# Kernel optimization log

Hardware: AMD Instinct MI355X
Metric: run time of the kernel (lower is better)

The kernel has to match this reference:

```python
import jax, jax.numpy as jnp
import numpy as np

EMBED_DIM = 1024
NUM_HEADS = 16
HEAD_DIM = EMBED_DIM // NUM_HEADS
B, L = 32, 2049
LN_EPS = 1e-5


def setup_inputs() -> dict:
    key = jax.random.key(0)
    ks = jax.random.split(key, 11)
    s = 1.0 / np.sqrt(EMBED_DIM)
    x = jax.random.normal(ks[0], (B, L, EMBED_DIM), dtype=jnp.float32)
    Wq = jax.random.normal(ks[1], (EMBED_DIM, EMBED_DIM), dtype=jnp.float32) * s
    bq = jnp.zeros((EMBED_DIM,), dtype=jnp.float32)
    Wk = jax.random.normal(ks[2], (EMBED_DIM, EMBED_DIM), dtype=jnp.float32) * s
    bk = jnp.zeros((EMBED_DIM,), dtype=jnp.float32)
    Wv = jax.random.normal(ks[3], (EMBED_DIM, EMBED_DIM), dtype=jnp.float32) * s
    bv = jnp.zeros((EMBED_DIM,), dtype=jnp.float32)
    Wo = jax.random.normal(ks[4], (EMBED_DIM, EMBED_DIM), dtype=jnp.float32) * s
    bo = jnp.zeros((EMBED_DIM,), dtype=jnp.float32)
    ln_g = jnp.ones((EMBED_DIM,), dtype=jnp.float32)
    ln_b = jnp.zeros((EMBED_DIM,), dtype=jnp.float32)
    return {"x": x, "Wq": Wq, "bq": bq, "Wk": Wk, "bk": bk, "Wv": Wv,
            "bv": bv, "Wo": Wo, "bo": bo, "ln_g": ln_g, "ln_b": ln_b}


def reference(x, Wq, bq, Wk, bk, Wv, bv, Wo, bo, ln_g, ln_b):
    # x: [B, L, D]; CLS token attends to the other L-1 tokens (dropout = eval/identity)
    cls_tok = x[:, 0, :]              # [B, D]
    others = x[:, 1:, :]              # [B, L-1, D]
    q = cls_tok @ Wq.T + bq           # [B, D]
    k = others @ Wk.T + bk            # [B, L-1, D]
    v = others @ Wv.T + bv            # [B, L-1, D]
    q = q.reshape(q.shape[0], NUM_HEADS, HEAD_DIM)                       # [B, H, d]
    k = k.reshape(k.shape[0], k.shape[1], NUM_HEADS, HEAD_DIM)           # [B, S, H, d]
    v = v.reshape(v.shape[0], v.shape[1], NUM_HEADS, HEAD_DIM)           # [B, S, H, d]
    scores = jnp.einsum('bhd,bshd->bhs', q, k) / np.sqrt(HEAD_DIM)       # [B, H, S]
    w = jax.nn.softmax(scores, axis=-1)
    attn = jnp.einsum('bhs,bshd->bhd', w, v)                             # [B, H, d]
    attn = attn.reshape(attn.shape[0], NUM_HEADS * HEAD_DIM)             # [B, D]
    out = attn @ Wo.T + bo
    y = out + cls_tok
    mu = jnp.mean(y, axis=-1, keepdims=True)
    var = jnp.var(y, axis=-1, keepdims=True)
    return (y - mu) / jnp.sqrt(var + LN_EPS) * ln_g + ln_b               # [B, D]
```

## Files before the change

### kernel.cpp

```cpp
#include <hip/hip_runtime.h>
#include <math.h>

#define B_ 32
#define L_ 2049
#define E_ 1024
#define H_ 16
#define NT_ 8
#define STILE 256
#define EC 32

#define OFF_Q     0
#define OFF_T     (OFF_Q + B_*E_)
#define OFF_QBK   (OFF_T + B_*H_*E_)
#define OFF_M     (OFF_QBK + B_*H_)
#define OFF_L     (OFF_M + B_*NT_*H_)
#define OFF_U     (OFF_L + B_*NT_*H_)
#define OFF_ATTN  (OFF_U + B_*H_*E_)
#define OFF_Y     (OFF_ATTN + B_*E_)
#define OFF_UP    (OFF_Y + B_*E_)

__global__ __launch_bounds__(256) void k_gemm32(const float* __restrict__ A, long long As, int mode,
                                                const float* __restrict__ W,
                                                const float* __restrict__ bias,
                                                const float* __restrict__ resid, long long Rs,
                                                float* __restrict__ C) {
    __shared__ float wls[2 * 1056];
    const int j0 = blockIdx.x * 2, tid = threadIdx.x;
    #pragma unroll
    for (int k = 0; k < 2; ++k) {
        int idx4 = k * 256 + tid;
        int row = idx4 >> 8, c4 = idx4 & 255;
        float4 v = *(const float4*)(W + (size_t)(j0 + row) * E_ + 4 * c4);
        *(float4*)&wls[row * 1056 + 4 * c4 + ((c4 >> 5) << 2)] = v;
    }
    __syncthreads();
    const int bb = tid >> 3, kseg = tid & 7;
    const long long kbase = (mode == 1) ? (long long)(j0 >> 6) * E_ : 0;
    const float* arow = A + (size_t)bb * As + kbase + kseg * 128;
    float a0 = 0.f, a1 = 0.f;
    #pragma unroll 4
    for (int i = 0; i < 32; ++i) {
        float4 av = *(const float4*)(arow + 4 * i);
        const float* wb = &wls[kseg * 132 + 4 * i];
        float4 w0 = *(const float4*)(wb);
        float4 w1 = *(const float4*)(wb + 1056);
        a0 += av.x * w0.x + av.y * w0.y + av.z * w0.z + av.w * w0.w;
        a1 += av.x * w1.x + av.y * w1.y + av.z * w1.z + av.w * w1.w;
    }
    #pragma unroll
    for (int off = 4; off; off >>= 1) {
        a0 += __shfl_down(a0, off, 8);
        a1 += __shfl_down(a1, off, 8);
    }
    if (kseg == 0) {
        float r0 = a0 + bias[j0], r1 = a1 + bias[j0 + 1];
        if (resid) {
            r0 += resid[(size_t)bb * Rs + j0];
            r1 += resid[(size_t)bb * Rs + j0 + 1];
        }
        C[(size_t)bb * E_ + j0] = r0;
        C[(size_t)bb * E_ + j0 + 1] = r1;
    }
}

__global__ __launch_bounds__(256) void k_tproj(const float* __restrict__ Wk,
                                               const float* __restrict__ bk,
                                               float* __restrict__ ws) {
    __shared__ float qs[64 * 33];
    __shared__ float wls[64 * 68];
    const int h = blockIdx.x, e0 = blockIdx.y * 64, tid = threadIdx.x;
    const float* q = ws + OFF_Q;
    #pragma unroll
    for (int k = 0; k < 8; ++k) {
        int idx = k * 256 + tid;
        int b = idx >> 6, d = idx & 63;
        qs[d * 33 + b] = q[(size_t)b * E_ + 64 * h + d];
    }
    #pragma unroll
    for (int k = 0; k < 4; ++k) {
        int idx4 = k * 256 + tid;
        int d = idx4 >> 4, c4 = idx4 & 15;
        float4 v = *(const float4*)(Wk + (size_t)(64 * h + d) * E_ + e0 + 4 * c4);
        *(float4*)&wls[d * 68 + 4 * c4] = v;
    }
    __syncthreads();
    const int el = tid & 63, bq8 = tid >> 6;
    float acc[8];
    #pragma unroll
    for (int i = 0; i < 8; ++i) acc[i] = 0.f;
    for (int d = 0; d < 64; ++d) {
        float wv = wls[d * 68 + el];
        #pragma unroll
        for (int i = 0; i < 8; ++i) acc[i] += qs[d * 33 + (bq8 * 8 + i)] * wv;
    }
    float* t = ws + OFF_T;
    #pragma unroll
    for (int i = 0; i < 8; ++i)
        t[((size_t)(bq8 * 8 + i) * H_ + h) * E_ + e0 + el] = acc[i] * 0.125f;
    if (e0 == 0 && tid < 32) {
        float s = 0.f;
        for (int d = 0; d < 64; ++d) s += qs[d * 33 + tid] * bk[64 * h + d];
        ws[OFF_QBK + tid * H_ + h] = s * 0.125f;
    }
}

__global__ __launch_bounds__(512) void k_attn_core(const float* __restrict__ x,
                                                   float* __restrict__ ws) {
    const int tile = blockIdx.x, b = blockIdx.y, tid = threadIdx.x;
    const int s0 = tile * STILE;
    const float* tmat = ws + OFF_T + (size_t)b * H_ * E_;
    const float* xb = x + (size_t)(b * L_ + 1 + s0) * E_;

    __shared__ float xs[18432];
    __shared__ float ts[1152];
    __shared__ float wl[STILE * 20];
    __shared__ float red[512];
    __shared__ float msh[16];

    const int lane = tid & 63;
    const int w = tid >> 6;

    float acc[16][4];
    #pragma unroll
    for (int hh = 0; hh < 16; ++hh)
        #pragma unroll
        for (int si = 0; si < 4; ++si) acc[hh][si] = 0.f;

    float4 xr[4];
    float tr;
    const int th = tid >> 5, te = tid & 31;
    {
        #pragma unroll
        for (int k = 0; k < 4; ++k) {
            int idx4 = k * 512 + tid, s = idx4 >> 3, e4 = idx4 & 7;
            xr[k] = *(const float4*)(xb + (size_t)s * E_ + 4 * e4);
        }
        tr = tmat[th * E_ + te];
        #pragma unroll
        for (int k = 0; k < 4; ++k) {
            int idx4 = k * 512 + tid, s = idx4 >> 3, e4 = idx4 & 7;
            *(float4*)&xs[s * 36 + 4 * e4] = xr[k];
        }
        ts[th * 36 + te] = tr;
    }
    for (int c = 0; c < 32; ++c) {
        __syncthreads();
        if (c + 1 < 32) {
            int ec = (c + 1) * EC;
            #pragma unroll
            for (int k = 0; k < 4; ++k) {
                int idx4 = k * 512 + tid, s = idx4 >> 3, e4 = idx4 & 7;
                xr[k] = *(const float4*)(xb + (size_t)s * E_ + ec + 4 * e4);
            }
            tr = tmat[th * E_ + ec + te];
        }
        const int bx = (c & 1) * 9216, bt = (c & 1) * 576;
        float4 xv[4];
        #pragma unroll
        for (int si = 0; si < 4; ++si)
            xv[si] = *(const float4*)&xs[bx + (lane + 64 * si) * 36 + 4 * w];
        #pragma unroll
        for (int hb = 0; hb < 4; ++hb) {
            float4 t0 = *(const float4*)&ts[bt + (4 * hb + 0) * 36 + 4 * w];
            float4 t1 = *(const float4*)&ts[bt + (4 * hb + 1) * 36 + 4 * w];
            float4 t2 = *(const float4*)&ts[bt + (4 * hb + 2) * 36 + 4 * w];
            float4 t3 = *(const float4*)&ts[bt + (4 * hb + 3) * 36 + 4 * w];
            #pragma unroll
            for (int si = 0; si < 4; ++si) {
                acc[4 * hb + 0][si] += t0.x * xv[si].x + t0.y * xv[si].y + t0.z * xv[si].z + t0.w * xv[si].w;
                acc[4 * hb + 1][si] += t1.x * xv[si].x + t1.y * xv[si].y + t1.z * xv[si].z + t1.w * xv[si].w;
                acc[4 * hb + 2][si] += t2.x * xv[si].x + t2.y * xv[si].y + t2.z * xv[si].z + t2.w * xv[si].w;
                acc[4 * hb + 3][si] += t3.x * xv[si].x + t3.y * xv[si].y + t3.z * xv[si].z + t3.w * xv[si].w;
            }
        }
        if (c + 1 < 32) {
            const int nx = ((c + 1) & 1) * 9216, nt = ((c + 1) & 1) * 576;
            #pragma unroll
            for (int k = 0; k < 4; ++k) {
                int idx4 = k * 512 + tid, s = idx4 >> 3, e4 = idx4 & 7;
                *(float4*)&xs[nx + s * 36 + 4 * e4] = xr[k];
            }
            ts[nt + th * 36 + te] = tr;
        }
    }
    __syncthreads();
    if (w >= 4) {
        float* pl = xs + (w - 4) * 4352;
        #pragma unroll
        for (int hh = 0; hh < 16; ++hh)
            #pragma unroll
            for (int si = 0; si < 4; ++si) pl[(lane + 64 * si) * 17 + hh] = acc[hh][si];
    }
    __syncthreads();
    if (w < 4) {
        const float* pl = xs + w * 4352;
        #pragma unroll
        for (int hh = 0; hh < 16; ++hh)
            #pragma unroll
            for (int si = 0; si < 4; ++si) acc[hh][si] += pl[(lane + 64 * si) * 17 + hh];
    }
    __syncthreads();
    if (w == 2 || w == 3) {
        float* pl = xs + (w - 2) * 4352;
        #pragma unroll
        for (int hh = 0; hh < 16; ++hh)
            #pragma unroll
            for (int si = 0; si < 4; ++si) pl[(lane + 64 * si) * 17 + hh] = acc[hh][si];
    }
    __syncthreads();
    if (w < 2) {
        const float* pl = xs + w * 4352;
        #pragma unroll
        for (int hh = 0; hh < 16; ++hh)
            #pragma unroll
            for (int si = 0; si < 4; ++si) acc[hh][si] += pl[(lane + 64 * si) * 17 + hh];
    }
    __syncthreads();
    if (w == 1) {
        float* pl = xs;
        #pragma unroll
        for (int hh = 0; hh < 16; ++hh)
            #pragma unroll
            for (int si = 0; si < 4; ++si) pl[(lane + 64 * si) * 17 + hh] = acc[hh][si];
    }
    __syncthreads();
    if (w == 0) {
        const float* pl = xs;
        const float* qbkp = ws + OFF_QBK + b * H_;
        #pragma unroll
        for (int hh = 0; hh < 16; ++hh) {
            float qb = qbkp[hh];
            #pragma unroll
            for (int si = 0; si < 4; ++si)
                wl[(lane + 64 * si) * 20 + hh] = acc[hh][si] + pl[(lane + 64 * si) * 17 + hh] + qb;
        }
    }
    __syncthreads();

    const int sh = tid & 15, seg = tid >> 4;
    {
        float m = -1e30f;
        #pragma unroll
        for (int i = 0; i < 8; ++i) m = fmaxf(m, wl[(seg * 8 + i) * 20 + sh]);
        red[seg * 16 + sh] = m;
    }
    __syncthreads();
    if (tid < 16) {
        float mm = -1e30f;
        for (int g = 0; g < 32; ++g) mm = fmaxf(mm, red[g * 16 + tid]);
        msh[tid] = mm;
    }
    __syncthreads();
    {
        float M = msh[sh];
        float ps = 0.f;
        #pragma unroll
        for (int i = 0; i < 8; ++i) {
            int idx = (seg * 8 + i) * 20 + sh;
            float v = __expf(wl[idx] - M);
            wl[idx] = v;
            ps += v;
        }
        __syncthreads();
        red[seg * 16 + sh] = ps;
    }
    __syncthreads();
    if (tid < 16) {
        float ss = 0.f;
        for (int g = 0; g < 32; ++g) ss += red[g * 16 + tid];
        ws[OFF_M + (b * NT_ + tile) * H_ + tid] = msh[tid];
        ws[OFF_L + (b * NT_ + tile) * H_ + tid] = ss;
    }

    float acc2[4][16];
    #pragma unroll
    for (int i = 0; i < 4; ++i)
        #pragma unroll
        for (int j = 0; j < 16; ++j) acc2[i][j] = 0.f;
    const int hq = 4 * (w & 3), rbase = 4 * (w >> 2);

    float4 xr2[4];
    #pragma unroll
    for (int k = 0; k < 4; ++k) {
        int idx4 = k * 512 + tid, r = idx4 >> 8, c4 = idx4 & 255;
        xr2[k] = *(const float4*)(xb + (size_t)r * E_ + 4 * c4);
    }
    __syncthreads();
    #pragma unroll
    for (int k = 0; k < 4; ++k) {
        int idx4 = k * 512 + tid, r = idx4 >> 8, c4 = idx4 & 255;
        *(float4*)&xs[r * 1028 + 4 * c4] = xr2[k];
    }
    for (int c = 0; c < 32; ++c) {
        __syncthreads();
        if (c + 1 < 32) {
            int sc = (c + 1) * 8;
            #pragma unroll
            for (int k = 0; k < 4; ++k) {
                int idx4 = k * 512 + tid, r = idx4 >> 8, c4 = idx4 & 255;
                xr2[k] = *(const float4*)(xb + (size_t)(sc + r) * E_ + 4 * c4);
            }
        }
        const int base = (c & 1) * 8224;
        #pragma unroll
        for (int rl = 0; rl < 4; ++rl) {
            const int r = rbase + rl;
            float4 wv = *(const float4*)&wl[(c * 8 + r) * 20 + hq];
            #pragma unroll
            for (int ej = 0; ej < 4; ++ej) {
                float4 xv = *(const float4*)&xs[base + r * 1028 + 4 * lane + 256 * ej];
                acc2[0][4 * ej + 0] += wv.x * xv.x; acc2[0][4 * ej + 1] += wv.x * xv.y;
                acc2[0][4 * ej + 2] += wv.x * xv.z; acc2[0][4 * ej + 3] += wv.x * xv.w;
                acc2[1][4 * ej + 0] += wv.y * xv.x; acc2[1][4 * ej + 1] += wv.y * xv.y;
                acc2[1][4 * ej + 2] += wv.y * xv.z; acc2[1][4 * ej + 3] += wv.y * xv.w;
                acc2[2][4 * ej + 0] += wv.z * xv.x; acc2[2][4 * ej + 1] += wv.z * xv.y;
                acc2[2][4 * ej + 2] += wv.z * xv.z; acc2[2][4 * ej + 3] += wv.z * xv.w;
                acc2[3][4 * ej + 0] += wv.w * xv.x; acc2[3][4 * ej + 1] += wv.w * xv.y;
                acc2[3][4 * ej + 2] += wv.w * xv.z; acc2[3][4 * ej + 3] += wv.w * xv.w;
            }
        }
        if (c + 1 < 32) {
            const int nb = ((c + 1) & 1) * 8224;
            #pragma unroll
            for (int k = 0; k < 4; ++k) {
                int idx4 = k * 512 + tid, r = idx4 >> 8, c4 = idx4 & 255;
                *(float4*)&xs[nb + r * 1028 + 4 * c4] = xr2[k];
            }
        }
    }
    __syncthreads();
    if (w >= 4) {
        const int qd = w & 3;
        #pragma unroll
        for (int hl = 0; hl < 4; ++hl)
            #pragma unroll
            for (int ej = 0; ej < 4; ++ej) {
                float4 o = make_float4(acc2[hl][4 * ej + 0], acc2[hl][4 * ej + 1],
                                       acc2[hl][4 * ej + 2], acc2[hl][4 * ej + 3]);
                *(float4*)&xs[qd * 4352 + hl * 1024 + 4 * lane + 256 * ej] = o;
            }
    }
    __syncthreads();
    if (w < 4) {
        float* up = ws + OFF_UP + (size_t)((b * NT_ + tile) * H_) * E_;
        #pragma unroll
        for (int hl = 0; hl < 4; ++hl)
            #pragma unroll
            for (int ej = 0; ej < 4; ++ej) {
                float4 pv = *(const float4*)&xs[w * 4352 + hl * 1024 + 4 * lane + 256 * ej];
                float4 o = make_float4(acc2[hl][4 * ej + 0] + pv.x, acc2[hl][4 * ej + 1] + pv.y,
                                       acc2[hl][4 * ej + 2] + pv.z, acc2[hl][4 * ej + 3] + pv.w);
                *(float4*)(up + (size_t)(hq + hl) * E_ + 4 * lane + 256 * ej) = o;
            }
    }
}

__global__ __launch_bounds__(256) void k_combine(float* __restrict__ ws) {
    const int b = blockIdx.x, h = blockIdx.y, tid = threadIdx.x;
    float m[NT_], l[NT_], f[NT_];
    float M = -1e30f;
    #pragma unroll
    for (int tg = 0; tg < NT_; ++tg) {
        m[tg] = ws[OFF_M + (b * NT_ + tg) * H_ + h];
        l[tg] = ws[OFF_L + (b * NT_ + tg) * H_ + h];
        M = fmaxf(M, m[tg]);
    }
    float Ls = 0.f;
    #pragma unroll
    for (int tg = 0; tg < NT_; ++tg) {
        f[tg] = __expf(m[tg] - M);
        Ls += f[tg] * l[tg];
    }
    const float inv = 1.f / Ls;
    float4 a = make_float4(0.f, 0.f, 0.f, 0.f);
    #pragma unroll
    for (int tg = 0; tg < NT_; ++tg) {
        float4 v = *(const float4*)(ws + OFF_UP + (size_t)((b * NT_ + tg) * H_ + h) * E_ + 4 * tid);
        a.x += f[tg] * v.x; a.y += f[tg] * v.y; a.z += f[tg] * v.z; a.w += f[tg] * v.w;
    }
    a.x *= inv; a.y *= inv; a.z *= inv; a.w *= inv;
    *(float4*)(ws + OFF_U + (size_t)(b * H_ + h) * E_ + 4 * tid) = a;
}

__global__ __launch_bounds__(256) void k_ln(const float* __restrict__ ws,
                                            const float* __restrict__ g,
                                            const float* __restrict__ be,
                                            float* __restrict__ out) {
    const int b = blockIdx.x, tid = threadIdx.x;
    const float* y = ws + OFF_Y + (size_t)b * E_;
    float4 v = *(const float4*)(y + 4 * tid);
    float s = v.x + v.y + v.z + v.w;
    float s2 = v.x * v.x + v.y * v.y + v.z * v.z + v.w * v.w;
    for (int o = 32; o; o >>= 1) {
        s += __shfl_down(s, o, 64);
        s2 += __shfl_down(s2, o, 64);
    }
    __shared__ float rs[4], rs2[4];
    int ww = tid >> 6;
    if ((tid & 63) == 0) { rs[ww] = s; rs2[ww] = s2; }
    __syncthreads();
    float S = rs[0] + rs[1] + rs[2] + rs[3];
    float S2 = rs2[0] + rs2[1] + rs2[2] + rs2[3];
    float mean = S * (1.f / 1024.f);
    float var = S2 * (1.f / 1024.f) - mean * mean;
    float r = rsqrtf(var + 1e-5f);
    float4 gv = *(const float4*)(g + 4 * tid);
    float4 bb2 = *(const float4*)(be + 4 * tid);
    float4 o;
    o.x = (v.x - mean) * r * gv.x + bb2.x;
    o.y = (v.y - mean) * r * gv.y + bb2.y;
    o.z = (v.z - mean) * r * gv.z + bb2.z;
    o.w = (v.w - mean) * r * gv.w + bb2.w;
    *(float4*)(out + (size_t)b * E_ + 4 * tid) = o;
}

extern "C" void kernel_launch(void* const* d_in, const int* in_sizes, int n_in,
                              void* d_out, int out_size, void* d_ws, size_t ws_size,
                              hipStream_t stream) {
    const float* x  = (const float*)d_in[0];
    const float* Wq = (const float*)d_in[1];
    const float* bq = (const float*)d_in[2];
    const float* Wk = (const float*)d_in[3];
    const float* bk = (const float*)d_in[4];
    const float* Wv = (const float*)d_in[5];
    const float* bv = (const float*)d_in[6];
    const float* Wo = (const float*)d_in[7];
    const float* bo = (const float*)d_in[8];
    const float* g  = (const float*)d_in[9];
    const float* be = (const float*)d_in[10];
    float* ws = (float*)d_ws;
    float* out = (float*)d_out;

    k_gemm32<<<512, 256, 0, stream>>>(x, (long long)L_ * E_, 0, Wq, bq, nullptr, 0, ws + OFF_Q);
    k_tproj<<<dim3(16, 16), 256, 0, stream>>>(Wk, bk, ws);
    k_attn_core<<<dim3(NT_, B_), 512, 0, stream>>>(x, ws);
    k_combine<<<dim3(B_, H_), 256, 0, stream>>>(ws);
    k_gemm32<<<512, 256, 0, stream>>>(ws + OFF_U, (long long)H_ * E_, 1, Wv, bv, nullptr, 0, ws + OFF_ATTN);
    k_gemm32<<<512, 256, 0, stream>>>(ws + OFF_ATTN, (long long)E_, 0, Wo, bo, x, (long long)L_ * E_, ws + OFF_Y);
    k_ln<<<B_, 256, 0, stream>>>(ws, g, be, out);
}
```

Baseline: 513.4 us.

## Restructure attention core: 1024-thread blocks, T matrix in LDS, direct x loads

The attention-core kernel now runs with 1024 threads per block and holds the whole per-batch 16x1024 T matrix in shared memory. Each thread reads its x rows straight from global memory for the score pass, so the per-chunk x staging through LDS goes away. Scores are reduced with wave shuffles instead of multi-stage LDS tree reductions, and the softmax max/sum uses shuffles plus a small shared array. The weighted-V pass is remapped so each thread handles two heads across half the rows, with a single cross-half reduction. The risks are uncoalesced strided global loads in the score pass and higher register pressure at 1024 threads.

```diff
diff --git a/kernel.cpp b/kernel.cpp
--- a/kernel.cpp
+++ b/kernel.cpp
@@ -7,7 +7,6 @@
 #define H_ 16
 #define NT_ 8
 #define STILE 256
-#define EC 32
 
 #define OFF_Q     0
 #define OFF_T     (OFF_Q + B_*E_)
@@ -104,254 +103,208 @@
     }
 }
 
-__global__ __launch_bounds__(512) void k_attn_core(const float* __restrict__ x,
-                                                   float* __restrict__ ws) {
+__global__ __launch_bounds__(1024, 4) void k_attn_core(const float* __restrict__ x,
+                                                       float* __restrict__ ws) {
     const int tile = blockIdx.x, b = blockIdx.y, tid = threadIdx.x;
-    const int s0 = tile * STILE;
+    const int s0t = tile * STILE;
     const float* tmat = ws + OFF_T + (size_t)b * H_ * E_;
-    const float* xb = x + (size_t)(b * L_ + 1 + s0) * E_;
-
-    __shared__ float xs[18432];
-    __shared__ float ts[1152];
-    __shared__ float wl[STILE * 20];
-    __shared__ float red[512];
-    __shared__ float msh[16];
-
-    const int lane = tid & 63;
-    const int w = tid >> 6;
-
-    float acc[16][4];
-    #pragma unroll
-    for (int hh = 0; hh < 16; ++hh)
-        #pragma unroll
-        for (int si = 0; si < 4; ++si) acc[hh][si] = 0.f;
-
-    float4 xr[4];
-    float tr;
-    const int th = tid >> 5, te = tid & 31;
+    const float* xb = x + (size_t)(b * L_ + 1 + s0t) * E_;
+
+    __shared__ float smem[16384];
+    __shared__ float wl[256 * 16];
+    __shared__ float pmax[128], psum[128], msh[16];
+
+    const int lane = tid & 63, w = tid >> 6;
+    const int g = lane & 3, ssub = lane >> 2;
+    const int wlo = w & 7;
+    const int ehalf = (w >> 3) * 512;
+    const int sA = 32 * wlo + ssub, sB = sA + 16;
+
+    #pragma unroll
+    for (int k = 0; k < 4; ++k) {
+        int idx4 = k * 1024 + tid;
+        *(float4*)&smem[4 * idx4] = *(const float4*)(tmat + 4 * idx4);
+    }
+    __syncthreads();
+
+    float acc[16][2];
+    #pragma unroll
+    for (int h = 0; h < 16; ++h) { acc[h][0] = 0.f; acc[h][1] = 0.f; }
+
     {
-        #pragma unroll
-        for (int k = 0; k < 4; ++k) {
-            int idx4 = k * 512 + tid, s = idx4 >> 3, e4 = idx4 & 7;
-            xr[k] = *(const float4*)(xb + (size_t)s * E_ + 4 * e4);
-        }
-        tr = tmat[th * E_ + te];
-        #pragma unroll
-        for (int k = 0; k < 4; ++k) {
-            int idx4 = k * 512 + tid, s = idx4 >> 3, e4 = idx4 & 7;
-            *(float4*)&xs[s * 36 + 4 * e4] = xr[k];
-        }
-        ts[th * 36 + te] = tr;
-    }
+        const float* xA = xb + (size_t)sA * E_ + ehalf + 8 * g;
+        const float* xB = xb + (size_t)sB * E_ + ehalf + 8 * g;
+        const float* tb = &smem[ehalf + 8 * g];
+        #pragma unroll 2
+        for (int c = 0; c < 16; ++c) {
+            float4 a0 = *(const float4*)(xA + 32 * c);
+            float4 a1 = *(const float4*)(xA + 32 * c + 4);
+            float4 b0 = *(const float4*)(xB + 32 * c);
+            float4 b1 = *(const float4*)(xB + 32 * c + 4);
+            #pragma unroll
+            for (int h = 0; h < 16; ++h) {
+                float4 t0 = *(const float4*)(tb + h * E_ + 32 * c);
+                float4 t1 = *(const float4*)(tb + h * E_ + 32 * c + 4);
+                acc[h][0] += t0.x * a0.x + t0.y * a0.y + t0.z * a0.z + t0.w * a0.w
+                           + t1.x * a1.x + t1.y * a1.y + t1.z * a1.z + t1.w * a1.w;
+                acc[h][1] += t0.x * b0.x + t0.y * b0.y + t0.z * b0.z + t0.w * b0.w
+                           + t1.x * b1.x + t1.y * b1.y + t1.z * b1.z + t1.w * b1.w;
+            }
+        }
+    }
+    #pragma unroll
+    for (int h = 0; h < 16; ++h) {
+        #pragma unroll
+        for (int s = 0; s < 2; ++s) {
+            float v = acc[h][s];
+            v += __shfl_xor(v, 1, 64);
+            v += __shfl_xor(v, 2, 64);
+            acc[h][s] = v;
+        }
+    }
+    if (w >= 8) {
+        if (g == 0) {
+            *(float4*)&wl[sA * 16 + 0]  = make_float4(acc[0][0], acc[1][0], acc[2][0], acc[3][0]);
+            *(float4*)&wl[sB * 16 + 0]  = make_float4(acc[0][1], acc[1][1], acc[2][1], acc[3][1]);
+        } else if (g == 1) {
+            *(float4*)&wl[sA * 16 + 4]  = make_float4(acc[4][0], acc[5][0], acc[6][0], acc[7][0]);
+            *(float4*)&wl[sB * 16 + 4]  = make_float4(acc[4][1], acc[5][1], acc[6][1], acc[7][1]);
+        } else if (g == 2) {
+            *(float4*)&wl[sA * 16 + 8]  = make_float4(acc[8][0], acc[9][0], acc[10][0], acc[11][0]);
+            *(float4*)&wl[sB * 16 + 8]  = make_float4(acc[8][1], acc[9][1], acc[10][1], acc[11][1]);
+        } else {
+            *(float4*)&wl[sA * 16 + 12] = make_float4(acc[12][0], acc[13][0], acc[14][0], acc[15][0]);
+            *(float4*)&wl[sB * 16 + 12] = make_float4(acc[12][1], acc[13][1], acc[14][1], acc[15][1]);
+        }
+    }
+    __syncthreads();
+
+    if (w < 8) {
+        const float* qbkp = ws + OFF_QBK + b * H_;
+        #pragma unroll
+        for (int h = 0; h < 16; ++h) {
+            float qb = qbkp[h];
+            acc[h][0] += wl[sA * 16 + h] + qb;
+            acc[h][1] += wl[sB * 16 + h] + qb;
+        }
+        #pragma unroll
+        for (int h = 0; h < 16; ++h) {
+            float v = fmaxf(acc[h][0], acc[h][1]);
+            v = fmaxf(v, __shfl_xor(v, 4, 64));
+            v = fmaxf(v, __shfl_xor(v, 8, 64));
+            v = fmaxf(v, __shfl_xor(v, 16, 64));
+            v = fmaxf(v, __shfl_xor(v, 32, 64));
+            if (lane == 0) pmax[w * 16 + h] = v;
+        }
+    }
+    __syncthreads();
+    if (tid < 16) {
+        float M = pmax[tid];
+        #pragma unroll
+        for (int q = 1; q < 8; ++q) M = fmaxf(M, pmax[q * 16 + tid]);
+        msh[tid] = M;
+        ws[OFF_M + (size_t)(b * NT_ + tile) * H_ + tid] = M;
+    }
+    __syncthreads();
+    if (w < 8) {
+        float ex0[16], ex1[16];
+        #pragma unroll
+        for (int h = 0; h < 16; ++h) {
+            float M = msh[h];
+            ex0[h] = __expf(acc[h][0] - M);
+            ex1[h] = __expf(acc[h][1] - M);
+        }
+        if (g == 0) {
+            *(float4*)&wl[sA * 16 + 0]  = make_float4(ex0[0], ex0[1], ex0[2], ex0[3]);
+            *(float4*)&wl[sB * 16 + 0]  = make_float4(ex1[0], ex1[1], ex1[2], ex1[3]);
+        } else if (g == 1) {
+            *(float4*)&wl[sA * 16 + 4]  = make_float4(ex0[4], ex0[5], ex0[6], ex0[7]);
+            *(float4*)&wl[sB * 16 + 4]  = make_float4(ex1[4], ex1[5], ex1[6], ex1[7]);
+        } else if (g == 2) {
+            *(float4*)&wl[sA * 16 + 8]  = make_float4(ex0[8], ex0[9], ex0[10], ex0[11]);
+            *(float4*)&wl[sB * 16 + 8]  = make_float4(ex1[8], ex1[9], ex1[10], ex1[11]);
+        } else {
+            *(float4*)&wl[sA * 16 + 12] = make_float4(ex0[12], ex0[13], ex0[14], ex0[15]);
+            *(float4*)&wl[sB * 16 + 12] = make_float4(ex1[12], ex1[13], ex1[14], ex1[15]);
+        }
+        #pragma unroll
+        for (int h = 0; h < 16; ++h) {
+            float v = ex0[h] + ex1[h];
+            v += __shfl_xor(v, 4, 64);
+            v += __shfl_xor(v, 8, 64);
+            v += __shfl_xor(v, 16, 64);
+            v += __shfl_xor(v, 32, 64);
+            if (lane == 0) psum[w * 16 + h] = v;
+        }
+    }
+    __syncthreads();
+    if (tid < 16) {
+        float Ls = 0.f;
+        #pragma unroll
+        for (int q = 0; q < 8; ++q) Ls += psum[q * 16 + tid];
+        ws[OFF_L + (size_t)(b * NT_ + tile) * H_ + tid] = Ls;
+    }
+
+    const int hp = w & 7, shalf = w >> 3;
+    float4 accA[4], accB[4];
+    #pragma unroll
+    for (int j = 0; j < 4; ++j) {
+        accA[j] = make_float4(0.f, 0.f, 0.f, 0.f);
+        accB[j] = make_float4(0.f, 0.f, 0.f, 0.f);
+    }
+    const int r0 = tid >> 8, c4 = tid & 255;
+    float4 st0 = *(const float4*)(xb + (size_t)(r0)     * E_ + 4 * c4);
+    float4 st1 = *(const float4*)(xb + (size_t)(r0 + 4) * E_ + 4 * c4);
+    *(float4*)&smem[(r0)     * 1024 + 4 * c4] = st0;
+    *(float4*)&smem[(r0 + 4) * 1024 + 4 * c4] = st1;
     for (int c = 0; c < 32; ++c) {
         __syncthreads();
         if (c + 1 < 32) {
-            int ec = (c + 1) * EC;
-            #pragma unroll
-            for (int k = 0; k < 4; ++k) {
-                int idx4 = k * 512 + tid, s = idx4 >> 3, e4 = idx4 & 7;
-                xr[k] = *(const float4*)(xb + (size_t)s * E_ + ec + 4 * e4);
-            }
-            tr = tmat[th * E_ + ec + te];
-        }
-        const int bx = (c & 1) * 9216, bt = (c & 1) * 576;
-        float4 xv[4];
-        #pragma unroll
-        for (int si = 0; si < 4; ++si)
-            xv[si] = *(const float4*)&xs[bx + (lane + 64 * si) * 36 + 4 * w];
-        #pragma unroll
-        for (int hb = 0; hb < 4; ++hb) {
-            float4 t0 = *(const float4*)&ts[bt + (4 * hb + 0) * 36 + 4 * w];
-            float4 t1 = *(const float4*)&ts[bt + (4 * hb + 1) * 36 + 4 * w];
-            float4 t2 = *(const float4*)&ts[bt + (4 * hb + 2) * 36 + 4 * w];
-            float4 t3 = *(const float4*)&ts[bt + (4 * hb + 3) * 36 + 4 * w];
-            #pragma unroll
-            for (int si = 0; si < 4; ++si) {
-                acc[4 * hb + 0][si] += t0.x * xv[si].x + t0.y * xv[si].y + t0.z * xv[si].z + t0.w * xv[si].w;
-                acc[4 * hb + 1][si] += t1.x * xv[si].x + t1.y * xv[si].y + t1.z * xv[si].z + t1.w * xv[si].w;
-                acc[4 * hb + 2][si] += t2.x * xv[si].x + t2.y * xv[si].y + t2.z * xv[si].z + t2.w * xv[si].w;
-                acc[4 * hb + 3][si] += t3.x * xv[si].x + t3.y * xv[si].y + t3.z * xv[si].z + t3.w * xv[si].w;
-            }
-        }
-        if (c + 1 < 32) {
-            const int nx = ((c + 1) & 1) * 9216, nt = ((c + 1) & 1) * 576;
-            #pragma unroll
-            for (int k = 0; k < 4; ++k) {
-                int idx4 = k * 512 + tid, s = idx4 >> 3, e4 = idx4 & 7;
-                *(float4*)&xs[nx + s * 36 + 4 * e4] = xr[k];
-            }
-            ts[nt + th * 36 + te] = tr;
-        }
-    }
-    __syncthreads();
-    if (w >= 4) {
-        float* pl = xs + (w - 4) * 4352;
-        #pragma unroll
-        for (int hh = 0; hh < 16; ++hh)
-            #pragma unroll
-            for (int si = 0; si < 4; ++si) pl[(lane + 64 * si) * 17 + hh] = acc[hh][si];
-    }
-    __syncthreads();
-    if (w < 4) {
-        const float* pl = xs + w * 4352;
-        #pragma unroll
-        for (int hh = 0; hh < 16; ++hh)
-            #pragma unroll
-            for (int si = 0; si < 4; ++si) acc[hh][si] += pl[(lane + 64 * si) * 17 + hh];
-    }
-    __syncthreads();
-    if (w == 2 || w == 3) {
-        float* pl = xs + (w - 2) * 4352;
-        #pragma unroll
-        for (int hh = 0; hh < 16; ++hh)
-            #pragma unroll
-            for (int si = 0; si < 4; ++si) pl[(lane + 64 * si) * 17 + hh] = acc[hh][si];
-    }
-    __syncthreads();
-    if (w < 2) {
-        const float* pl = xs + w * 4352;
-        #pragma unroll
-        for (int hh = 0; hh < 16; ++hh)
-            #pragma unroll
-            for (int si = 0; si < 4; ++si) acc[hh][si] += pl[(lane + 64 * si) * 17 + hh];
-    }
-    __syncthreads();
-    if (w == 1) {
-        float* pl = xs;
-        #pragma unroll
-        for (int hh = 0; hh < 16; ++hh)
-            #pragma unroll
-            for (int si = 0; si < 4; ++si) pl[(lane + 64 * si) * 17 + hh] = acc[hh][si];
-    }
-    __syncthreads();
-    if (w == 0) {
-        const float* pl = xs;
-        const float* qbkp = ws + OFF_QBK + b * H_;
-        #pragma unroll
-        for (int hh = 0; hh < 16; ++hh) {
-            float qb = qbkp[hh];
-            #pragma unroll
-            for (int si = 0; si < 4; ++si)
-                wl[(lane + 64 * si) * 20 + hh] = acc[hh][si] + pl[(lane + 64 * si) * 17 + hh] + qb;
-        }
-    }
-    __syncthreads();
-
-    const int sh = tid & 15, seg = tid >> 4;
-    {
-        float m = -1e30f;
-        #pragma unroll
-        for (int i = 0; i < 8; ++i) m = fmaxf(m, wl[(seg * 8 + i) * 20 + sh]);
-        red[seg * 16 + sh] = m;
-    }
-    __syncthreads();
-    if (tid < 16) {
-        float mm = -1e30f;
-        for (int g = 0; g < 32; ++g) mm = fmaxf(mm, red[g * 16 + tid]);
-        msh[tid] = mm;
-    }
-    __syncthreads();
-    {
-        float M = msh[sh];
-        float ps = 0.f;
-        #pragma unroll
-        for (int i = 0; i < 8; ++i) {
-            int idx = (seg * 8 + i) * 20 + sh;
-            float v = __expf(wl[idx] - M);
-            wl[idx] = v;
-            ps += v;
-        }
-        __syncthreads();
-        red[seg * 16 + sh] = ps;
-    }
-    __syncthreads();
-    if (tid < 16) {
-        float ss = 0.f;
-        for (int g = 0; g < 32; ++g) ss += red[g * 16 + tid];
-        ws[OFF_M + (b * NT_ + tile) * H_ + tid] = msh[tid];
-        ws[OFF_L + (b * NT_ + tile) * H_ + tid] = ss;
-    }
-
-    float acc2[4][16];
-    #pragma unroll
-    for (int i = 0; i < 4; ++i)
-        #pragma unroll
-        for (int j = 0; j < 16; ++j) acc2[i][j] = 0.f;
-    const int hq = 4 * (w & 3), rbase = 4 * (w >> 2);
-
-    float4 xr2[4];
-    #pragma unroll
-    for (int k = 0; k < 4; ++k) {
-        int idx4 = k * 512 + tid, r = idx4 >> 8, c4 = idx4 & 255;
-        xr2[k] = *(const float4*)(xb + (size_t)r * E_ + 4 * c4);
-    }
-    __syncthreads();
-    #pragma unroll
-    for (int k = 0; k < 4; ++k) {
-        int idx4 = k * 512 + tid, r = idx4 >> 8, c4 = idx4 & 255;
-        *(float4*)&xs[r * 1028 + 4 * c4] = xr2[k];
-    }
-    for (int c = 0; c < 32; ++c) {
-        __syncthreads();
-        if (c + 1 < 32) {
-            int sc = (c + 1) * 8;
-            #pragma unroll
-            for (int k = 0; k < 4; ++k) {
-                int idx4 = k * 512 + tid, r = idx4 >> 8, c4 = idx4 & 255;
-                xr2[k] = *(const float4*)(xb + (size_t)(sc + r) * E_ + 4 * c4);
-            }
-        }
-        const int base = (c & 1) * 8224;
-        #pragma unroll
-        for (int rl = 0; rl < 4; ++rl) {
-            const int r = rbase + rl;
-            float4 wv = *(const float4*)&wl[(c * 8 + r) * 20 + hq];
+            st0 = *(const float4*)(xb + (size_t)(8 * (c + 1) + r0)     * E_ + 4 * c4);
+            st1 = *(const float4*)(xb + (size_t)(8 * (c + 1) + r0 + 4) * E_ + 4 * c4);
+        }
+        const float* A = &smem[(c & 1) * 8192];
+        #pragma unroll
+        for (int rr = 0; rr < 4; ++rr) {
+            const int r = 4 * shalf + rr;
+            float2 wv = *(const float2*)&wl[(8 * c + r) * 16 + 2 * hp];
             #pragma unroll
             for (int ej = 0; ej < 4; ++ej) {
-                float4 xv = *(const float4*)&xs[base + r * 1028 + 4 * lane + 256 * ej];
-                acc2[0][4 * ej + 0] += wv.x * xv.x; acc2[0][4 * ej + 1] += wv.x * xv.y;
-                acc2[0][4 * ej + 2] += wv.x * xv.z; acc2[0][4 * ej + 3] += wv.x * xv.w;
-                acc2[1][4 * ej + 0] += wv.y * xv.x; acc2[1][4 * ej + 1] += wv.y * xv.y;
-                acc2[1][4 * ej + 2] += wv.y * xv.z; acc2[1][4 * ej + 3] += wv.y * xv.w;
-                acc2[2][4 * ej + 0] += wv.z * xv.x; acc2[2][4 * ej + 1] += wv.z * xv.y;
-                acc2[2][4 * ej + 2] += wv.z * xv.z; acc2[2][4 * ej + 3] += wv.z * xv.w;
-                acc2[3][4 * ej + 0] += wv.w * xv.x; acc2[3][4 * ej + 1] += wv.w * xv.y;
-                acc2[3][4 * ej + 2] += wv.w * xv.z; acc2[3][4 * ej + 3] += wv.w * xv.w;
+                float4 xv = *(const float4*)&A[r * 1024 + 4 * lane + 256 * ej];
+                accA[ej].x += wv.x * xv.x; accA[ej].y += wv.x * xv.y;
+                accA[ej].z += wv.x * xv.z; accA[ej].w += wv.x * xv.w;
+                accB[ej].x += wv.y * xv.x; accB[ej].y += wv.y * xv.y;
+                accB[ej].z += wv.y * xv.z; accB[ej].w += wv.y * xv.w;
             }
         }
         if (c + 1 < 32) {
-            const int nb = ((c + 1) & 1) * 8224;
-            #pragma unroll
-            for (int k = 0; k < 4; ++k) {
-                int idx4 = k * 512 + tid, r = idx4 >> 8, c4 = idx4 & 255;
-                *(float4*)&xs[nb + r * 1028 + 4 * c4] = xr2[k];
-            }
-        }
-    }
-    __syncthreads();
-    if (w >= 4) {
-        const int qd = w & 3;
-        #pragma unroll
-        for (int hl = 0; hl < 4; ++hl)
-            #pragma unroll
-            for (int ej = 0; ej < 4; ++ej) {
-                float4 o = make_float4(acc2[hl][4 * ej + 0], acc2[hl][4 * ej + 1],
-                                       acc2[hl][4 * ej + 2], acc2[hl][4 * ej + 3]);
-                *(float4*)&xs[qd * 4352 + hl * 1024 + 4 * lane + 256 * ej] = o;
-            }
-    }
-    __syncthreads();
-    if (w < 4) {
-        float* up = ws + OFF_UP + (size_t)((b * NT_ + tile) * H_) * E_;
-        #pragma unroll
-        for (int hl = 0; hl < 4; ++hl)
-            #pragma unroll
-            for (int ej = 0; ej < 4; ++ej) {
-                float4 pv = *(const float4*)&xs[w * 4352 + hl * 1024 + 4 * lane + 256 * ej];
-                float4 o = make_float4(acc2[hl][4 * ej + 0] + pv.x, acc2[hl][4 * ej + 1] + pv.y,
-                                       acc2[hl][4 * ej + 2] + pv.z, acc2[hl][4 * ej + 3] + pv.w);
-                *(float4*)(up + (size_t)(hq + hl) * E_ + 4 * lane + 256 * ej) = o;
-            }
+            float* D = &smem[((c + 1) & 1) * 8192];
+            *(float4*)&D[(r0)     * 1024 + 4 * c4] = st0;
+            *(float4*)&D[(r0 + 4) * 1024 + 4 * c4] = st1;
+        }
+    }
+    __syncthreads();
+    if (shalf == 1) {
+        #pragma unroll
+        for (int ej = 0; ej < 4; ++ej) {
+            *(float4*)&smem[hp * 2048 +        4 * lane + 256 * ej] = accA[ej];
+            *(float4*)&smem[hp * 2048 + 1024 + 4 * lane + 256 * ej] = accB[ej];
+        }
+    }
+    __syncthreads();
+    if (shalf == 0) {
+        float* up = ws + OFF_UP + ((size_t)(b * NT_ + tile) * H_ + 2 * hp) * E_;
+        #pragma unroll
+        for (int ej = 0; ej < 4; ++ej) {
+            float4 pA = *(const float4*)&smem[hp * 2048 +        4 * lane + 256 * ej];
+            float4 pB = *(const float4*)&smem[hp * 2048 + 1024 + 4 * lane + 256 * ej];
+            float4 oA = make_float4(accA[ej].x + pA.x, accA[ej].y + pA.y,
+                                    accA[ej].z + pA.z, accA[ej].w + pA.w);
+            float4 oB = make_float4(accB[ej].x + pB.x, accB[ej].y + pB.y,
+                                    accB[ej].z + pB.z, accB[ej].w + pB.w);
+            *(float4*)(up +       4 * lane + 256 * ej) = oA;
+            *(float4*)(up + E_ +  4 * lane + 256 * ej) = oB;
+        }
     }
 }
 
@@ -433,7 +386,7 @@
 
     k_gemm32<<<512, 256, 0, stream>>>(x, (long long)L_ * E_, 0, Wq, bq, nullptr, 0, ws + OFF_Q);
     k_tproj<<<dim3(16, 16), 256, 0, stream>>>(Wk, bk, ws);
-    k_attn_core<<<dim3(NT_, B_), 512, 0, stream>>>(x, ws);
+    k_attn_core<<<dim3(NT_, B_), 1024, 0, stream>>>(x, ws);
     k_combine<<<dim3(B_, H_), 256, 0, stream>>>(ws);
     k_gemm32<<<512, 256, 0, stream>>>(ws + OFF_U, (long long)H_ * E_, 1, Wv, bv, nullptr, 0, ws + OFF_ATTN);
     k_gemm32<<<512, 256, 0, stream>>>(ws + OFF_ATTN, (long long)E_, 0, Wo, bo, x, (long long)L_ * E_, ws + OFF_Y);
```

New measurement: 727.5 us. 1.42x slower.
